# Optimization experiments

Hardware: AMD Instinct MI355X
Metric: run time of the kernel (lower is better)

## Reference

```python
import jax, jax.numpy as jnp
import numpy as np

N = 50000        # nodes
E = 1_600_000    # edges (avg degree 32)
IN_DIM = 128
NUM_CONFS = 16
CONF_EMB = 4
HIDDEN = 64
OUT = 32


def setup_inputs() -> dict:
    key = jax.random.key(0)
    ks = jax.random.split(key, 8)
    x = jax.random.normal(ks[0], (N, IN_DIM), jnp.float32)
    conf_ids = jax.random.randint(ks[1], (N,), 0, NUM_CONFS)
    edge_index = jax.random.randint(ks[2], (2, E), 0, N)
    edge_weight = jax.random.uniform(ks[3], (E,), jnp.float32)
    # learned params
    conf_table = jax.random.normal(ks[4], (NUM_CONFS, CONF_EMB), jnp.float32) * 0.1
    W1 = jax.random.normal(ks[5], (IN_DIM + CONF_EMB, HIDDEN), jnp.float32) / np.sqrt(IN_DIM + CONF_EMB)
    b1 = jnp.zeros((HIDDEN,), jnp.float32)
    W2 = jax.random.normal(ks[6], (HIDDEN, OUT), jnp.float32) / np.sqrt(HIDDEN)
    b2 = jnp.zeros((OUT,), jnp.float32)
    return dict(x=x, conf_ids=conf_ids, edge_index=edge_index, edge_weight=edge_weight,
                conf_table=conf_table, W1=W1, b1=b1, W2=W2, b2=b2)


def _gcn_conv(h, W, b, row, col, w, n):
    """PyG GCNConv: symmetric norm with self-loops (loops already appended to row/col/w)."""
    deg = jax.ops.segment_sum(w, col, num_segments=n)              # weighted in-degree [N]
    dinv = jnp.where(deg > 0, jax.lax.rsqrt(deg), 0.0)             # D^{-1/2}
    norm = dinv[row] * w * dinv[col]                               # per-edge coefficient [E+N]
    hW = h @ W                                                     # [N, out]
    out = jax.ops.segment_sum(hW[row] * norm[:, None], col, num_segments=n)
    return out + b


def reference(x, conf_ids, edge_index, edge_weight, conf_table, W1, b1, W2, b2):
    row, col = edge_index[0], edge_index[1]
    # add self-loops once (same math for both conv layers)
    loop = jnp.arange(N)
    row = jnp.concatenate([row, loop])
    col = jnp.concatenate([col, loop])
    w = jnp.concatenate([edge_weight, jnp.ones((N,), edge_weight.dtype)])

    h = jnp.concatenate([x, conf_table[conf_ids]], axis=-1)        # [N, in+conf_emb]
    h = jax.nn.relu(_gcn_conv(h, W1, b1, row, col, w, N))
    return _gcn_conv(h, W2, b2, row, col, w, N)
```

## Files before the change

### kernel.cpp

```cpp
#include <hip/hip_runtime.h>
#include <hip/hip_fp16.h>

#define BKT_SHIFT 8
#define BKT_SIZE  256
#define SEGCAP    12544
#define EPB       4096
#define EPT       16
#define NTX       64

__global__ void k_zero(int* __restrict__ cursor) {
    cursor[threadIdx.x] = 0;
}

__global__ void k_binA(const int* __restrict__ row, const int* __restrict__ col,
                       const float* __restrict__ w, int* __restrict__ cursor,
                       uint2* __restrict__ seg, int e) {
    __shared__ int hist[256];
    __shared__ int begL[256];
    __shared__ int gbase[256];
    __shared__ int rank[256];
    __shared__ uint2 pay[EPB];
    int t = threadIdx.x;
    hist[t] = 0; rank[t] = 0;
    __syncthreads();
    int b0 = blockIdx.x * EPB;
    int cnt_local = min(EPB, e - b0);
    unsigned pv[EPT]; unsigned cc[EPT];
#pragma unroll
    for (int k = 0; k < EPT; ++k) {
        int i = b0 + k * 256 + t;
        if (i < e) {
            unsigned r  = (unsigned)row[i];
            unsigned c  = (unsigned)col[i];
            unsigned wq = (unsigned)__half_as_ushort(__float2half_rn(w[i]));
            pv[k] = r | (wq << 16);
            cc[k] = c;
            atomicAdd(&hist[c >> BKT_SHIFT], 1);
        } else cc[k] = 0xFFFFFFFFu;
    }
    __syncthreads();
    int v = hist[t];
    begL[t] = v;
    __syncthreads();
    for (int off = 1; off < 256; off <<= 1) {
        int tv = (t >= off) ? begL[t - off] : 0;
        __syncthreads();
        begL[t] += tv;
        __syncthreads();
    }
    int excl = begL[t] - v;
    __syncthreads();
    begL[t] = excl;
    if (v > 0) gbase[t] = atomicAdd(&cursor[t], v);
    __syncthreads();
#pragma unroll
    for (int k = 0; k < EPT; ++k) {
        if (cc[k] != 0xFFFFFFFFu) {
            int b = cc[k] >> BKT_SHIFT;
            int pos = begL[b] + atomicAdd(&rank[b], 1);
            pay[pos] = make_uint2(pv[k], ((unsigned)b << 8) | (cc[k] & (BKT_SIZE - 1)));
        }
    }
    __syncthreads();
    for (int i = t; i < cnt_local; i += 256) {
        uint2 r = pay[i];
        int b = r.y >> 8;
        int gidx = gbase[b] + (i - begL[b]);
        if (gidx < SEGCAP)
            seg[(size_t)b * SEGCAP + gidx] = make_uint2(r.x, r.y & (BKT_SIZE - 1));
    }
}

__global__ void k_binB(const int* __restrict__ cursor, const uint2* __restrict__ seg,
                       unsigned* __restrict__ csr, int* __restrict__ begs,
                       int* __restrict__ cnts, float* __restrict__ dinv, int n) {
    __shared__ int hist[BKT_SIZE];
    __shared__ float wsumf[BKT_SIZE];
    __shared__ int begL[BKT_SIZE];
    __shared__ int rank[BKT_SIZE];
    __shared__ unsigned pay[SEGCAP];
    int b = blockIdx.x;
    int t = threadIdx.x;
    int nodes = min(BKT_SIZE, n - b * BKT_SIZE);
    int count = min(cursor[b], SEGCAP);
    hist[t] = 0; wsumf[t] = 0.f; rank[t] = 0;
    __syncthreads();
    const uint2* sp = seg + (size_t)b * SEGCAP;
    for (int i = t; i < count; i += 256) {
        uint2 r = sp[i];
        atomicAdd(&hist[r.y], 1);
        atomicAdd(&wsumf[r.y], __half2float(__ushort_as_half((unsigned short)(r.x >> 16))));
    }
    __syncthreads();
    int v = hist[t];
    int vpad = (v + 15) & ~15;
    begL[t] = vpad;
    __syncthreads();
    for (int off = 1; off < 256; off <<= 1) {
        int tv = (t >= off) ? begL[t - off] : 0;
        __syncthreads();
        begL[t] += tv;
        __syncthreads();
    }
    int beg_excl = begL[t] - vpad;
    int ptot = min(begL[255], SEGCAP);
    __syncthreads();
    begL[t] = beg_excl;
    if (t < nodes) {
        int node = b * BKT_SIZE + t;
        begs[node] = b * SEGCAP + beg_excl;
        cnts[node] = vpad;
        dinv[node] = rsqrtf(1.0f + wsumf[t]);
    }
    for (int i = t; i < ptot; i += 256) pay[i] = 0u;
    __syncthreads();
    for (int i = t; i < count; i += 256) {
        uint2 r = sp[i];
        int pos = begL[r.y] + atomicAdd(&rank[r.y], 1);
        if (pos < SEGCAP) pay[pos] = r.x;
    }
    __syncthreads();
    unsigned* cp = csr + (size_t)b * SEGCAP;
    for (int i = t; i < ptot; i += 256) cp[i] = pay[i];
}

__global__ void k_hw1(const float* __restrict__ x, const int* __restrict__ conf_ids,
                      const float* __restrict__ conf_table, const float* __restrict__ W1,
                      const float* __restrict__ dinv, __half* __restrict__ hW1s, int n) {
    __shared__ float xs[NTX][132];
    int t = threadIdx.x;
    int base = blockIdx.x * NTX;
    for (int q = t; q < NTX * 32; q += 256) {
        int node = base + (q >> 5);
        int k4 = (q & 31) * 4;
        float4 v = make_float4(0.f, 0.f, 0.f, 0.f);
        if (node < n) v = *(const float4*)(x + (size_t)node * 128 + k4);
        *(float4*)&xs[q >> 5][k4] = v;
    }
    if (t < NTX) {
        int node = base + t;
        int cid = (node < n) ? conf_ids[node] : 0;
        float4 ce = *(const float4*)(conf_table + cid * 4);
        if (node >= n) ce = make_float4(0.f, 0.f, 0.f, 0.f);
        *(float4*)&xs[t][128] = ce;
    }
    __syncthreads();
    int w = t >> 6;
    int lane = t & 63;
    int fbase = __builtin_amdgcn_readfirstlane(w * 16);
    const float* __restrict__ wp = W1 + fbase;
    float acc[16];
#pragma unroll
    for (int j = 0; j < 16; ++j) acc[j] = 0.f;
    for (int k4 = 0; k4 < 132; k4 += 4) {
        float4 xv = *(const float4*)&xs[lane][k4];
#pragma unroll
        for (int j = 0; j < 16; ++j) {
            acc[j] += xv.x * wp[(k4 + 0) * 64 + j]
                    + xv.y * wp[(k4 + 1) * 64 + j]
                    + xv.z * wp[(k4 + 2) * 64 + j]
                    + xv.w * wp[(k4 + 3) * 64 + j];
        }
    }
    int node = base + lane;
    if (node < n) {
        float dn = dinv[node];
        half2* hp = (half2*)(hW1s + (size_t)node * 64 + fbase);
#pragma unroll
        for (int j = 0; j < 8; ++j)
            hp[j] = __floats2half2_rn(acc[2 * j] * dn, acc[2 * j + 1] * dn);
    }
}

__global__ void k_agg1(const __half* __restrict__ hW1s, const int* __restrict__ begs,
                       const int* __restrict__ cnts, const unsigned* __restrict__ csr,
                       const float* __restrict__ dinv, const float* __restrict__ b1,
                       const float* __restrict__ W2, __half* __restrict__ hW2s, int n) {
    __shared__ float h1s[8][64];
    int t = threadIdx.x;
    int q  = t >> 5;
    int hl = t & 31;
    int nid = blockIdx.x * 8 + q;
    const half2* __restrict__ hrow = (const half2*)hW1s;
    float dn = 0.f;
    float2 sf = make_float2(0.f, 0.f);
    int c = 0;
    const unsigned* sp = csr;
    if (nid < n) {
        dn = dinv[nid];
        c = cnts[nid];
        sp = csr + begs[nid];
        sf = __half22float2(hrow[(size_t)nid * 32 + hl]);
    }
    float a0 = 0.f, a1 = 0.f;
    const half2 hz = __float2half2_rn(0.f);
    uint4 s0 = *(const uint4*)(sp);
    uint4 s1 = *(const uint4*)(sp + 4);
    uint4 s2 = *(const uint4*)(sp + 8);
    uint4 s3 = *(const uint4*)(sp + 12);
    for (int j = 0; j < c; j += 16) {
        uint4 n0 = *(const uint4*)(sp + j + 16);
        uint4 n1 = *(const uint4*)(sp + j + 20);
        uint4 n2 = *(const uint4*)(sp + j + 24);
        uint4 n3 = *(const uint4*)(sp + j + 28);
        half2 acc0 = hz, acc1 = hz, acc2 = hz, acc3 = hz;
#define STEP1(s, A) { half2 vv = hrow[(size_t)((s) & 0xffffu) * 32 + hl]; \
                      half2 ww = __half2half2(__ushort_as_half((unsigned short)((s) >> 16))); \
                      A = __hfma2(vv, ww, A); }
        STEP1(s0.x, acc0) STEP1(s0.y, acc1) STEP1(s0.z, acc2) STEP1(s0.w, acc3)
        STEP1(s1.x, acc0) STEP1(s1.y, acc1) STEP1(s1.z, acc2) STEP1(s1.w, acc3)
        STEP1(s2.x, acc0) STEP1(s2.y, acc1) STEP1(s2.z, acc2) STEP1(s2.w, acc3)
        STEP1(s3.x, acc0) STEP1(s3.y, acc1) STEP1(s3.z, acc2) STEP1(s3.w, acc3)
#undef STEP1
        float2 f0 = __half22float2(acc0);
        float2 f1 = __half22float2(acc1);
        float2 f2 = __half22float2(acc2);
        float2 f3 = __half22float2(acc3);
        a0 += (f0.x + f1.x) + (f2.x + f3.x);
        a1 += (f0.y + f1.y) + (f2.y + f3.y);
        s0 = n0; s1 = n1; s2 = n2; s3 = n3;
    }
    float2 bb = *(const float2*)(b1 + 2 * hl);
    float h0  = fmaxf((sf.x + a0) * dn + bb.x, 0.0f);
    float h1v = fmaxf((sf.y + a1) * dn + bb.y, 0.0f);
    if (nid >= n) { h0 = 0.f; h1v = 0.f; }
    *(float2*)&h1s[q][2 * hl] = make_float2(h0, h1v);
    __syncthreads();
    float s = 0.f;
#pragma unroll
    for (int k = 0; k < 64; k += 4) {
        float4 hv = *(const float4*)&h1s[q][k];
        s += hv.x * W2[(k + 0) * 32 + hl];
        s += hv.y * W2[(k + 1) * 32 + hl];
        s += hv.z * W2[(k + 2) * 32 + hl];
        s += hv.w * W2[(k + 3) * 32 + hl];
    }
    if (nid < n) hW2s[(size_t)nid * 32 + hl] = __float2half_rn(s * dn);
}

__global__ void k_agg2(const __half* __restrict__ hW2s, const int* __restrict__ begs,
                       const int* __restrict__ cnts, const unsigned* __restrict__ csr,
                       const float* __restrict__ dinv, const float* __restrict__ b2,
                       float* __restrict__ out, int n) {
    int t = threadIdx.x;
    int g  = t >> 4;
    int hl = t & 15;
    int nid = blockIdx.x * 16 + g;
    const half2* __restrict__ hrow = (const half2*)hW2s;
    float dn = 0.f;
    float2 sf = make_float2(0.f, 0.f);
    int c = 0;
    const unsigned* sp = csr;
    if (nid < n) {
        dn = dinv[nid];
        c = cnts[nid];
        sp = csr + begs[nid];
        sf = __half22float2(hrow[(size_t)nid * 16 + hl]);
    }
    float a0 = 0.f, a1 = 0.f;
    const half2 hz = __float2half2_rn(0.f);
    uint4 s0 = *(const uint4*)(sp);
    uint4 s1 = *(const uint4*)(sp + 4);
    uint4 s2 = *(const uint4*)(sp + 8);
    uint4 s3 = *(const uint4*)(sp + 12);
    for (int j = 0; j < c; j += 16) {
        uint4 n0 = *(const uint4*)(sp + j + 16);
        uint4 n1 = *(const uint4*)(sp + j + 20);
        uint4 n2 = *(const uint4*)(sp + j + 24);
        uint4 n3 = *(const uint4*)(sp + j + 28);
        half2 acc0 = hz, acc1 = hz, acc2 = hz, acc3 = hz;
#define STEP2(s, A) { half2 vv = hrow[(size_t)((s) & 0xffffu) * 16 + hl]; \
                      half2 ww = __half2half2(__ushort_as_half((unsigned short)((s) >> 16))); \
                      A = __hfma2(vv, ww, A); }
        STEP2(s0.x, acc0) STEP2(s0.y, acc1) STEP2(s0.z, acc2) STEP2(s0.w, acc3)
        STEP2(s1.x, acc0) STEP2(s1.y, acc1) STEP2(s1.z, acc2) STEP2(s1.w, acc3)
        STEP2(s2.x, acc0) STEP2(s2.y, acc1) STEP2(s2.z, acc2) STEP2(s2.w, acc3)
        STEP2(s3.x, acc0) STEP2(s3.y, acc1) STEP2(s3.z, acc2) STEP2(s3.w, acc3)
#undef STEP2
        float2 f0 = __half22float2(acc0);
        float2 f1 = __half22float2(acc1);
        float2 f2 = __half22float2(acc2);
        float2 f3 = __half22float2(acc3);
        a0 += (f0.x + f1.x) + (f2.x + f3.x);
        a1 += (f0.y + f1.y) + (f2.y + f3.y);
        s0 = n0; s1 = n1; s2 = n2; s3 = n3;
    }
    if (nid < n) {
        float2 bb = *(const float2*)(b2 + 2 * hl);
        float o0 = (sf.x + a0) * dn + bb.x;
        float o1 = (sf.y + a1) * dn + bb.y;
        *(float2*)&out[(size_t)nid * 32 + 2 * hl] = make_float2(o0, o1);
    }
}

extern "C" void kernel_launch(void* const* d_in, const int* in_sizes, int n_in,
                              void* d_out, int out_size, void* d_ws, size_t ws_size,
                              hipStream_t stream) {
    const float* x          = (const float*)d_in[0];
    const int*   conf_ids   = (const int*)  d_in[1];
    const int*   eidx       = (const int*)  d_in[2];
    const float* ew         = (const float*)d_in[3];
    const float* conf_table = (const float*)d_in[4];
    const float* W1         = (const float*)d_in[5];
    const float* b1         = (const float*)d_in[6];
    const float* W2         = (const float*)d_in[7];
    const float* b2         = (const float*)d_in[8];
    float* out = (float*)d_out;

    const int n = in_sizes[1];
    const int e = in_sizes[3];
    const int* row = eidx;
    const int* col = eidx + e;
    const int nbkt = (n + BKT_SIZE - 1) / BKT_SIZE;

    char* ws = (char*)d_ws;
    size_t off = 0;
    auto alloc = [&](size_t bytes) -> char* {
        char* p = ws + off;
        off = (off + bytes + 255) & ~(size_t)255;
        return p;
    };
    int*      cursor = (int*)     alloc(256 * 4);
    uint2*    seg    = (uint2*)   alloc((size_t)nbkt * SEGCAP * 8);
    unsigned* csr    = (unsigned*)alloc((size_t)nbkt * SEGCAP * 4);
    int*      begs   = (int*)     alloc((size_t)n * 4);
    int*      cnts   = (int*)     alloc((size_t)n * 4);
    float*    dinv   = (float*)   alloc((size_t)n * 4);
    __half*   hW2s   = (__half*)  alloc((size_t)n * 32 * 2);
    __half*   hW1s   = (__half*)  alloc((size_t)n * 64 * 2);

    const int B = 256;
    int ga  = (e + EPB - 1) / EPB;
    int gt  = (n + NTX - 1) / NTX;
    int g8  = (n + 7) / 8;
    int g16 = (n + 15) / 16;

    k_zero<<<1,    B, 0, stream>>>(cursor);
    k_binA<<<ga,   B, 0, stream>>>(row, col, ew, cursor, seg, e);
    k_binB<<<nbkt, B, 0, stream>>>(cursor, seg, csr, begs, cnts, dinv, n);
    k_hw1 <<<gt,   B, 0, stream>>>(x, conf_ids, conf_table, W1, dinv, hW1s, n);
    k_agg1<<<g8,   B, 0, stream>>>(hW1s, begs, cnts, csr, dinv, b1, W2, hW2s, n);
    k_agg2<<<g16,  B, 0, stream>>>(hW2s, begs, cnts, csr, dinv, b2, out, n);
}
```

Before: 121.6 us.

## Run X·W1 GEMM concurrently with edge binning and apply dinv scaling in binB

Merges the edge-binning kernel and the dense X·W1 kernel into one launch, with blocks split by blockIdx, so the GEMM no longer waits for degree computation and can overlap with binning. The dinv row scaling moves into k_binB, which rescales the unscaled fp16 hW1 rows of its bucket after computing dinv. This removes one launch and the serial dependency, but adds an extra read-modify-write pass over hW1 and a second fp16 rounding step. The shared-memory union sizes each block to the larger of the two layouts, which may lower occupancy for the GEMM blocks.

```diff
diff --git a/kernel.cpp b/kernel.cpp
--- a/kernel.cpp
+++ b/kernel.cpp
@@ -12,68 +12,116 @@
     cursor[threadIdx.x] = 0;
 }
 
-__global__ void k_binA(const int* __restrict__ row, const int* __restrict__ col,
-                       const float* __restrict__ w, int* __restrict__ cursor,
-                       uint2* __restrict__ seg, int e) {
-    __shared__ int hist[256];
-    __shared__ int begL[256];
-    __shared__ int gbase[256];
-    __shared__ int rank[256];
-    __shared__ uint2 pay[EPB];
+struct ShA { int hist[256]; int begL[256]; int gbase[256]; int rank[256]; uint2 pay[EPB]; };
+struct ShH { float xs[NTX][132]; };
+
+__global__ void k_binA_hw1(const int* __restrict__ row, const int* __restrict__ col,
+                           const float* __restrict__ w, int* __restrict__ cursor,
+                           uint2* __restrict__ seg,
+                           const float* __restrict__ x, const int* __restrict__ conf_ids,
+                           const float* __restrict__ conf_table, const float* __restrict__ W1,
+                           __half* __restrict__ hW1, int e, int n, int ga) {
+    __shared__ __align__(16) char raw[sizeof(ShA) > sizeof(ShH) ? sizeof(ShA) : sizeof(ShH)];
     int t = threadIdx.x;
-    hist[t] = 0; rank[t] = 0;
-    __syncthreads();
-    int b0 = blockIdx.x * EPB;
-    int cnt_local = min(EPB, e - b0);
-    unsigned pv[EPT]; unsigned cc[EPT];
-#pragma unroll
-    for (int k = 0; k < EPT; ++k) {
-        int i = b0 + k * 256 + t;
-        if (i < e) {
-            unsigned r  = (unsigned)row[i];
-            unsigned c  = (unsigned)col[i];
-            unsigned wq = (unsigned)__half_as_ushort(__float2half_rn(w[i]));
-            pv[k] = r | (wq << 16);
-            cc[k] = c;
-            atomicAdd(&hist[c >> BKT_SHIFT], 1);
-        } else cc[k] = 0xFFFFFFFFu;
-    }
-    __syncthreads();
-    int v = hist[t];
-    begL[t] = v;
-    __syncthreads();
-    for (int off = 1; off < 256; off <<= 1) {
-        int tv = (t >= off) ? begL[t - off] : 0;
-        __syncthreads();
-        begL[t] += tv;
-        __syncthreads();
-    }
-    int excl = begL[t] - v;
-    __syncthreads();
-    begL[t] = excl;
-    if (v > 0) gbase[t] = atomicAdd(&cursor[t], v);
-    __syncthreads();
-#pragma unroll
-    for (int k = 0; k < EPT; ++k) {
-        if (cc[k] != 0xFFFFFFFFu) {
-            int b = cc[k] >> BKT_SHIFT;
-            int pos = begL[b] + atomicAdd(&rank[b], 1);
-            pay[pos] = make_uint2(pv[k], ((unsigned)b << 8) | (cc[k] & (BKT_SIZE - 1)));
-        }
-    }
-    __syncthreads();
-    for (int i = t; i < cnt_local; i += 256) {
-        uint2 r = pay[i];
-        int b = r.y >> 8;
-        int gidx = gbase[b] + (i - begL[b]);
-        if (gidx < SEGCAP)
-            seg[(size_t)b * SEGCAP + gidx] = make_uint2(r.x, r.y & (BKT_SIZE - 1));
+    if ((int)blockIdx.x < ga) {
+        ShA& A = *reinterpret_cast<ShA*>(raw);
+        A.hist[t] = 0; A.rank[t] = 0;
+        __syncthreads();
+        int b0 = blockIdx.x * EPB;
+        int cnt_local = min(EPB, e - b0);
+        unsigned pv[EPT]; unsigned cc[EPT];
+#pragma unroll
+        for (int k = 0; k < EPT; ++k) {
+            int i = b0 + k * 256 + t;
+            if (i < e) {
+                unsigned r  = (unsigned)row[i];
+                unsigned c  = (unsigned)col[i];
+                unsigned wq = (unsigned)__half_as_ushort(__float2half_rn(w[i]));
+                pv[k] = r | (wq << 16);
+                cc[k] = c;
+                atomicAdd(&A.hist[c >> BKT_SHIFT], 1);
+            } else cc[k] = 0xFFFFFFFFu;
+        }
+        __syncthreads();
+        int v = A.hist[t];
+        A.begL[t] = v;
+        __syncthreads();
+        for (int off = 1; off < 256; off <<= 1) {
+            int tv = (t >= off) ? A.begL[t - off] : 0;
+            __syncthreads();
+            A.begL[t] += tv;
+            __syncthreads();
+        }
+        int excl = A.begL[t] - v;
+        __syncthreads();
+        A.begL[t] = excl;
+        if (v > 0) A.gbase[t] = atomicAdd(&cursor[t], v);
+        __syncthreads();
+#pragma unroll
+        for (int k = 0; k < EPT; ++k) {
+            if (cc[k] != 0xFFFFFFFFu) {
+                int b = cc[k] >> BKT_SHIFT;
+                int pos = A.begL[b] + atomicAdd(&A.rank[b], 1);
+                A.pay[pos] = make_uint2(pv[k], ((unsigned)b << 8) | (cc[k] & (BKT_SIZE - 1)));
+            }
+        }
+        __syncthreads();
+        for (int i = t; i < cnt_local; i += 256) {
+            uint2 r = A.pay[i];
+            int b = r.y >> 8;
+            int gidx = A.gbase[b] + (i - A.begL[b]);
+            if (gidx < SEGCAP)
+                seg[(size_t)b * SEGCAP + gidx] = make_uint2(r.x, r.y & (BKT_SIZE - 1));
+        }
+    } else {
+        ShH& H = *reinterpret_cast<ShH*>(raw);
+        int base = (blockIdx.x - ga) * NTX;
+        for (int q = t; q < NTX * 32; q += 256) {
+            int node = base + (q >> 5);
+            int k4 = (q & 31) * 4;
+            float4 v = make_float4(0.f, 0.f, 0.f, 0.f);
+            if (node < n) v = *(const float4*)(x + (size_t)node * 128 + k4);
+            *(float4*)&H.xs[q >> 5][k4] = v;
+        }
+        if (t < NTX) {
+            int node = base + t;
+            int cid = (node < n) ? conf_ids[node] : 0;
+            float4 ce = *(const float4*)(conf_table + cid * 4);
+            if (node >= n) ce = make_float4(0.f, 0.f, 0.f, 0.f);
+            *(float4*)&H.xs[t][128] = ce;
+        }
+        __syncthreads();
+        int wv = t >> 6;
+        int lane = t & 63;
+        int fbase = __builtin_amdgcn_readfirstlane(wv * 16);
+        const float* __restrict__ wp = W1 + fbase;
+        float acc[16];
+#pragma unroll
+        for (int j = 0; j < 16; ++j) acc[j] = 0.f;
+        for (int k4 = 0; k4 < 132; k4 += 4) {
+            float4 xv = *(const float4*)&H.xs[lane][k4];
+#pragma unroll
+            for (int j = 0; j < 16; ++j) {
+                acc[j] += xv.x * wp[(k4 + 0) * 64 + j]
+                        + xv.y * wp[(k4 + 1) * 64 + j]
+                        + xv.z * wp[(k4 + 2) * 64 + j]
+                        + xv.w * wp[(k4 + 3) * 64 + j];
+            }
+        }
+        int node = base + lane;
+        if (node < n) {
+            half2* hp = (half2*)(hW1 + (size_t)node * 64 + fbase);
+#pragma unroll
+            for (int j = 0; j < 8; ++j)
+                hp[j] = __floats2half2_rn(acc[2 * j], acc[2 * j + 1]);
+        }
     }
 }
 
 __global__ void k_binB(const int* __restrict__ cursor, const uint2* __restrict__ seg,
                        unsigned* __restrict__ csr, int* __restrict__ begs,
-                       int* __restrict__ cnts, float* __restrict__ dinv, int n) {
+                       int* __restrict__ cnts, float* __restrict__ dinv,
+                       __half* __restrict__ hW1, int n) {
     __shared__ int hist[BKT_SIZE];
     __shared__ float wsumf[BKT_SIZE];
     __shared__ int begL[BKT_SIZE];
@@ -106,11 +154,14 @@
     int ptot = min(begL[255], SEGCAP);
     __syncthreads();
     begL[t] = beg_excl;
+    float dv = rsqrtf(1.0f + wsumf[t]);
+    __syncthreads();
+    wsumf[t] = dv;
     if (t < nodes) {
         int node = b * BKT_SIZE + t;
         begs[node] = b * SEGCAP + beg_excl;
         cnts[node] = vpad;
-        dinv[node] = rsqrtf(1.0f + wsumf[t]);
+        dinv[node] = dv;
     }
     for (int i = t; i < ptot; i += 256) pay[i] = 0u;
     __syncthreads();
@@ -122,53 +173,12 @@
     __syncthreads();
     unsigned* cp = csr + (size_t)b * SEGCAP;
     for (int i = t; i < ptot; i += 256) cp[i] = pay[i];
-}
-
-__global__ void k_hw1(const float* __restrict__ x, const int* __restrict__ conf_ids,
-                      const float* __restrict__ conf_table, const float* __restrict__ W1,
-                      const float* __restrict__ dinv, __half* __restrict__ hW1s, int n) {
-    __shared__ float xs[NTX][132];
-    int t = threadIdx.x;
-    int base = blockIdx.x * NTX;
-    for (int q = t; q < NTX * 32; q += 256) {
-        int node = base + (q >> 5);
-        int k4 = (q & 31) * 4;
-        float4 v = make_float4(0.f, 0.f, 0.f, 0.f);
-        if (node < n) v = *(const float4*)(x + (size_t)node * 128 + k4);
-        *(float4*)&xs[q >> 5][k4] = v;
-    }
-    if (t < NTX) {
-        int node = base + t;
-        int cid = (node < n) ? conf_ids[node] : 0;
-        float4 ce = *(const float4*)(conf_table + cid * 4);
-        if (node >= n) ce = make_float4(0.f, 0.f, 0.f, 0.f);
-        *(float4*)&xs[t][128] = ce;
-    }
-    __syncthreads();
-    int w = t >> 6;
-    int lane = t & 63;
-    int fbase = __builtin_amdgcn_readfirstlane(w * 16);
-    const float* __restrict__ wp = W1 + fbase;
-    float acc[16];
-#pragma unroll
-    for (int j = 0; j < 16; ++j) acc[j] = 0.f;
-    for (int k4 = 0; k4 < 132; k4 += 4) {
-        float4 xv = *(const float4*)&xs[lane][k4];
-#pragma unroll
-        for (int j = 0; j < 16; ++j) {
-            acc[j] += xv.x * wp[(k4 + 0) * 64 + j]
-                    + xv.y * wp[(k4 + 1) * 64 + j]
-                    + xv.z * wp[(k4 + 2) * 64 + j]
-                    + xv.w * wp[(k4 + 3) * 64 + j];
-        }
-    }
-    int node = base + lane;
-    if (node < n) {
-        float dn = dinv[node];
-        half2* hp = (half2*)(hW1s + (size_t)node * 64 + fbase);
-#pragma unroll
-        for (int j = 0; j < 8; ++j)
-            hp[j] = __floats2half2_rn(acc[2 * j] * dn, acc[2 * j + 1] * dn);
+    half2* hp = (half2*)(hW1 + (size_t)b * BKT_SIZE * 64);
+    int lim = nodes * 32;
+    for (int i = t; i < lim; i += 256) {
+        float dn = wsumf[i >> 5];
+        float2 f = __half22float2(hp[i]);
+        hp[i] = __floats2half2_rn(f.x * dn, f.y * dn);
     }
 }
 
@@ -327,7 +337,7 @@
     int*      cnts   = (int*)     alloc((size_t)n * 4);
     float*    dinv   = (float*)   alloc((size_t)n * 4);
     __half*   hW2s   = (__half*)  alloc((size_t)n * 32 * 2);
-    __half*   hW1s   = (__half*)  alloc((size_t)n * 64 * 2);
+    __half*   hW1    = (__half*)  alloc((size_t)n * 64 * 2);
 
     const int B = 256;
     int ga  = (e + EPB - 1) / EPB;
@@ -335,10 +345,10 @@
     int g8  = (n + 7) / 8;
     int g16 = (n + 15) / 16;
 
-    k_zero<<<1,    B, 0, stream>>>(cursor);
-    k_binA<<<ga,   B, 0, stream>>>(row, col, ew, cursor, seg, e);
-    k_binB<<<nbkt, B, 0, stream>>>(cursor, seg, csr, begs, cnts, dinv, n);
-    k_hw1 <<<gt,   B, 0, stream>>>(x, conf_ids, conf_table, W1, dinv, hW1s, n);
-    k_agg1<<<g8,   B, 0, stream>>>(hW1s, begs, cnts, csr, dinv, b1, W2, hW2s, n);
-    k_agg2<<<g16,  B, 0, stream>>>(hW2s, begs, cnts, csr, dinv, b2, out, n);
-}
+    k_zero    <<<1,       B, 0, stream>>>(cursor);
+    k_binA_hw1<<<ga + gt, B, 0, stream>>>(row, col, ew, cursor, seg,
+                                          x, conf_ids, conf_table, W1, hW1, e, n, ga);
+    k_binB    <<<nbkt,    B, 0, stream>>>(cursor, seg, csr, begs, cnts, dinv, hW1, n);
+    k_agg1    <<<g8,      B, 0, stream>>>(hW1, begs, cnts, csr, dinv, b1, W2, hW2s, n);
+    k_agg2    <<<g16,     B, 0, stream>>>(hW2s, begs, cnts, csr, dinv, b2, out, n);
+}
```

Result: no change. 122.8 us (+1.0%).

## Reorder dense transform before binning, pad cursors, use wave-shuffle scan in binA

Applied to the files above, without the earlier changes.

k_hw1 now runs before k_binB and no longer depends on dinv. k_binB applies the dinv scaling to hW1 in place, which breaks the dependency and gives more freedom in kernel ordering. binA now uses half the edges per block to launch more blocks, and its block scan uses wave shuffles instead of barrier loops. The global cursor counters are spread out with a stride so that contended atomics sit on separate cache lines. The cost is an extra read and write of hW1 inside binB, and the pairs rounding twice to fp16.

```diff
diff --git a/kernel.cpp b/kernel.cpp
--- a/kernel.cpp
+++ b/kernel.cpp
@@ -4,12 +4,13 @@
 #define BKT_SHIFT 8
 #define BKT_SIZE  256
 #define SEGCAP    12544
-#define EPB       4096
-#define EPT       16
+#define EPB       2048
+#define EPT       8
 #define NTX       64
+#define CSTR      32
 
 __global__ void k_zero(int* __restrict__ cursor) {
-    cursor[threadIdx.x] = 0;
+    for (int i = threadIdx.x; i < 256 * CSTR; i += 256) cursor[i] = 0;
 }
 
 __global__ void k_binA(const int* __restrict__ row, const int* __restrict__ col,
@@ -19,6 +20,7 @@
     __shared__ int begL[256];
     __shared__ int gbase[256];
     __shared__ int rank[256];
+    __shared__ int wsum[4];
     __shared__ uint2 pay[EPB];
     int t = threadIdx.x;
     hist[t] = 0; rank[t] = 0;
@@ -40,18 +42,21 @@
     }
     __syncthreads();
     int v = hist[t];
-    begL[t] = v;
-    __syncthreads();
-    for (int off = 1; off < 256; off <<= 1) {
-        int tv = (t >= off) ? begL[t - off] : 0;
-        __syncthreads();
-        begL[t] += tv;
-        __syncthreads();
-    }
-    int excl = begL[t] - v;
-    __syncthreads();
+    int lane = t & 63, wid = t >> 6;
+    int s = v;
+#pragma unroll
+    for (int off = 1; off < 64; off <<= 1) {
+        int u = __shfl_up(s, off);
+        if (lane >= off) s += u;
+    }
+    if (lane == 63) wsum[wid] = s;
+    __syncthreads();
+    int pre = 0;
+#pragma unroll
+    for (int k = 0; k < 4; ++k) if (k < wid) pre += wsum[k];
+    int excl = s + pre - v;
     begL[t] = excl;
-    if (v > 0) gbase[t] = atomicAdd(&cursor[t], v);
+    if (v > 0) gbase[t] = atomicAdd(&cursor[t * CSTR], v);
     __syncthreads();
 #pragma unroll
     for (int k = 0; k < EPT; ++k) {
@@ -71,62 +76,9 @@
     }
 }
 
-__global__ void k_binB(const int* __restrict__ cursor, const uint2* __restrict__ seg,
-                       unsigned* __restrict__ csr, int* __restrict__ begs,
-                       int* __restrict__ cnts, float* __restrict__ dinv, int n) {
-    __shared__ int hist[BKT_SIZE];
-    __shared__ float wsumf[BKT_SIZE];
-    __shared__ int begL[BKT_SIZE];
-    __shared__ int rank[BKT_SIZE];
-    __shared__ unsigned pay[SEGCAP];
-    int b = blockIdx.x;
-    int t = threadIdx.x;
-    int nodes = min(BKT_SIZE, n - b * BKT_SIZE);
-    int count = min(cursor[b], SEGCAP);
-    hist[t] = 0; wsumf[t] = 0.f; rank[t] = 0;
-    __syncthreads();
-    const uint2* sp = seg + (size_t)b * SEGCAP;
-    for (int i = t; i < count; i += 256) {
-        uint2 r = sp[i];
-        atomicAdd(&hist[r.y], 1);
-        atomicAdd(&wsumf[r.y], __half2float(__ushort_as_half((unsigned short)(r.x >> 16))));
-    }
-    __syncthreads();
-    int v = hist[t];
-    int vpad = (v + 15) & ~15;
-    begL[t] = vpad;
-    __syncthreads();
-    for (int off = 1; off < 256; off <<= 1) {
-        int tv = (t >= off) ? begL[t - off] : 0;
-        __syncthreads();
-        begL[t] += tv;
-        __syncthreads();
-    }
-    int beg_excl = begL[t] - vpad;
-    int ptot = min(begL[255], SEGCAP);
-    __syncthreads();
-    begL[t] = beg_excl;
-    if (t < nodes) {
-        int node = b * BKT_SIZE + t;
-        begs[node] = b * SEGCAP + beg_excl;
-        cnts[node] = vpad;
-        dinv[node] = rsqrtf(1.0f + wsumf[t]);
-    }
-    for (int i = t; i < ptot; i += 256) pay[i] = 0u;
-    __syncthreads();
-    for (int i = t; i < count; i += 256) {
-        uint2 r = sp[i];
-        int pos = begL[r.y] + atomicAdd(&rank[r.y], 1);
-        if (pos < SEGCAP) pay[pos] = r.x;
-    }
-    __syncthreads();
-    unsigned* cp = csr + (size_t)b * SEGCAP;
-    for (int i = t; i < ptot; i += 256) cp[i] = pay[i];
-}
-
 __global__ void k_hw1(const float* __restrict__ x, const int* __restrict__ conf_ids,
                       const float* __restrict__ conf_table, const float* __restrict__ W1,
-                      const float* __restrict__ dinv, __half* __restrict__ hW1s, int n) {
+                      __half* __restrict__ hW1, int n) {
     __shared__ float xs[NTX][132];
     int t = threadIdx.x;
     int base = blockIdx.x * NTX;
@@ -145,9 +97,9 @@
         *(float4*)&xs[t][128] = ce;
     }
     __syncthreads();
-    int w = t >> 6;
+    int wv = t >> 6;
     int lane = t & 63;
-    int fbase = __builtin_amdgcn_readfirstlane(w * 16);
+    int fbase = __builtin_amdgcn_readfirstlane(wv * 16);
     const float* __restrict__ wp = W1 + fbase;
     float acc[16];
 #pragma unroll
@@ -164,11 +116,74 @@
     }
     int node = base + lane;
     if (node < n) {
-        float dn = dinv[node];
-        half2* hp = (half2*)(hW1s + (size_t)node * 64 + fbase);
+        half2* hp = (half2*)(hW1 + (size_t)node * 64 + fbase);
 #pragma unroll
         for (int j = 0; j < 8; ++j)
-            hp[j] = __floats2half2_rn(acc[2 * j] * dn, acc[2 * j + 1] * dn);
+            hp[j] = __floats2half2_rn(acc[2 * j], acc[2 * j + 1]);
+    }
+}
+
+__global__ void k_binB(const int* __restrict__ cursor, const uint2* __restrict__ seg,
+                       unsigned* __restrict__ csr, int* __restrict__ begs,
+                       int* __restrict__ cnts, float* __restrict__ dinv,
+                       __half* __restrict__ hW1, int n) {
+    __shared__ int hist[BKT_SIZE];
+    __shared__ float wsumf[BKT_SIZE];
+    __shared__ int begL[BKT_SIZE];
+    __shared__ int rank[BKT_SIZE];
+    __shared__ unsigned pay[SEGCAP];
+    int b = blockIdx.x;
+    int t = threadIdx.x;
+    int nodes = min(BKT_SIZE, n - b * BKT_SIZE);
+    int count = min(cursor[b * CSTR], SEGCAP);
+    hist[t] = 0; wsumf[t] = 0.f; rank[t] = 0;
+    __syncthreads();
+    const uint2* sp = seg + (size_t)b * SEGCAP;
+    for (int i = t; i < count; i += 256) {
+        uint2 r = sp[i];
+        atomicAdd(&hist[r.y], 1);
+        atomicAdd(&wsumf[r.y], __half2float(__ushort_as_half((unsigned short)(r.x >> 16))));
+    }
+    __syncthreads();
+    int v = hist[t];
+    int vpad = (v + 15) & ~15;
+    begL[t] = vpad;
+    __syncthreads();
+    for (int off = 1; off < 256; off <<= 1) {
+        int tv = (t >= off) ? begL[t - off] : 0;
+        __syncthreads();
+        begL[t] += tv;
+        __syncthreads();
+    }
+    int beg_excl = begL[t] - vpad;
+    int ptot = min(begL[255], SEGCAP);
+    __syncthreads();
+    begL[t] = beg_excl;
+    float dv = rsqrtf(1.0f + wsumf[t]);
+    __syncthreads();
+    wsumf[t] = dv;
+    if (t < nodes) {
+        int node = b * BKT_SIZE + t;
+        begs[node] = b * SEGCAP + beg_excl;
+        cnts[node] = vpad;
+        dinv[node] = dv;
+    }
+    for (int i = t; i < ptot; i += 256) pay[i] = 0u;
+    __syncthreads();
+    for (int i = t; i < count; i += 256) {
+        uint2 r = sp[i];
+        int pos = begL[r.y] + atomicAdd(&rank[r.y], 1);
+        if (pos < SEGCAP) pay[pos] = r.x;
+    }
+    __syncthreads();
+    unsigned* cp = csr + (size_t)b * SEGCAP;
+    for (int i = t; i < ptot; i += 256) cp[i] = pay[i];
+    half2* hp = (half2*)(hW1 + (size_t)b * BKT_SIZE * 64);
+    int lim = nodes * 32;
+    for (int i = t; i < lim; i += 256) {
+        float dn = wsumf[i >> 5];
+        float2 f = __half22float2(hp[i]);
+        hp[i] = __floats2half2_rn(f.x * dn, f.y * dn);
     }
 }
 
@@ -320,14 +335,14 @@
         off = (off + bytes + 255) & ~(size_t)255;
         return p;
     };
-    int*      cursor = (int*)     alloc(256 * 4);
+    int*      cursor = (int*)     alloc(256 * CSTR * 4);
     uint2*    seg    = (uint2*)   alloc((size_t)nbkt * SEGCAP * 8);
     unsigned* csr    = (unsigned*)alloc((size_t)nbkt * SEGCAP * 4);
     int*      begs   = (int*)     alloc((size_t)n * 4);
     int*      cnts   = (int*)     alloc((size_t)n * 4);
     float*    dinv   = (float*)   alloc((size_t)n * 4);
     __half*   hW2s   = (__half*)  alloc((size_t)n * 32 * 2);
-    __half*   hW1s   = (__half*)  alloc((size_t)n * 64 * 2);
+    __half*   hW1    = (__half*)  alloc((size_t)n * 64 * 2);
 
     const int B = 256;
     int ga  = (e + EPB - 1) / EPB;
@@ -337,8 +352,8 @@
 
     k_zero<<<1,    B, 0, stream>>>(cursor);
     k_binA<<<ga,   B, 0, stream>>>(row, col, ew, cursor, seg, e);
-    k_binB<<<nbkt, B, 0, stream>>>(cursor, seg, csr, begs, cnts, dinv, n);
-    k_hw1 <<<gt,   B, 0, stream>>>(x, conf_ids, conf_table, W1, dinv, hW1s, n);
-    k_agg1<<<g8,   B, 0, stream>>>(hW1s, begs, cnts, csr, dinv, b1, W2, hW2s, n);
+    k_hw1 <<<gt,   B, 0, stream>>>(x, conf_ids, conf_table, W1, hW1, n);
+    k_binB<<<nbkt, B, 0, stream>>>(cursor, seg, csr, begs, cnts, dinv, hW1, n);
+    k_agg1<<<g8,   B, 0, stream>>>(hW1, begs, cnts, csr, dinv, b1, W2, hW2s, n);
     k_agg2<<<g16,  B, 0, stream>>>(hW2s, begs, cnts, csr, dinv, b2, out, n);
 }
```

Result: slower. 126.9 us (+4.4%).

## Fuse cursor zeroing into hW1 GEMM and apply dinv scaling inside binB

Applied to the files above, without the earlier changes.

Moves the feature transform x·W1 to the start of the pipeline, merged with cursor zeroing, so it no longer depends on dinv and the separate k_zero launch goes away. The dinv row scaling is applied afterwards in k_binB, which reads back each bucket's hW1 rows, scales them and rewrites them in fp16. This removes one kernel launch but adds an extra read-modify-write pass over hW1 and rounds to fp16 twice.

```diff
diff --git a/kernel.cpp b/kernel.cpp
--- a/kernel.cpp
+++ b/kernel.cpp
@@ -8,8 +8,52 @@
 #define EPT       16
 #define NTX       64
 
-__global__ void k_zero(int* __restrict__ cursor) {
-    cursor[threadIdx.x] = 0;
+__global__ void k_hw1z(const float* __restrict__ x, const int* __restrict__ conf_ids,
+                       const float* __restrict__ conf_table, const float* __restrict__ W1,
+                       __half* __restrict__ hW1, int* __restrict__ cursor, int n) {
+    __shared__ float xs[NTX][132];
+    int t = threadIdx.x;
+    if (blockIdx.x == 0) cursor[t] = 0;
+    int base = blockIdx.x * NTX;
+    for (int q = t; q < NTX * 32; q += 256) {
+        int node = base + (q >> 5);
+        int k4 = (q & 31) * 4;
+        float4 v = make_float4(0.f, 0.f, 0.f, 0.f);
+        if (node < n) v = *(const float4*)(x + (size_t)node * 128 + k4);
+        *(float4*)&xs[q >> 5][k4] = v;
+    }
+    if (t < NTX) {
+        int node = base + t;
+        int cid = (node < n) ? conf_ids[node] : 0;
+        float4 ce = *(const float4*)(conf_table + cid * 4);
+        if (node >= n) ce = make_float4(0.f, 0.f, 0.f, 0.f);
+        *(float4*)&xs[t][128] = ce;
+    }
+    __syncthreads();
+    int wv = t >> 6;
+    int lane = t & 63;
+    int fbase = __builtin_amdgcn_readfirstlane(wv * 16);
+    const float* __restrict__ wp = W1 + fbase;
+    float acc[16];
+#pragma unroll
+    for (int j = 0; j < 16; ++j) acc[j] = 0.f;
+    for (int k4 = 0; k4 < 132; k4 += 4) {
+        float4 xv = *(const float4*)&xs[lane][k4];
+#pragma unroll
+        for (int j = 0; j < 16; ++j) {
+            acc[j] += xv.x * wp[(k4 + 0) * 64 + j]
+                    + xv.y * wp[(k4 + 1) * 64 + j]
+                    + xv.z * wp[(k4 + 2) * 64 + j]
+                    + xv.w * wp[(k4 + 3) * 64 + j];
+        }
+    }
+    int node = base + lane;
+    if (node < n) {
+        half2* hp = (half2*)(hW1 + (size_t)node * 64 + fbase);
+#pragma unroll
+        for (int j = 0; j < 8; ++j)
+            hp[j] = __floats2half2_rn(acc[2 * j], acc[2 * j + 1]);
+    }
 }
 
 __global__ void k_binA(const int* __restrict__ row, const int* __restrict__ col,
@@ -73,7 +117,8 @@
 
 __global__ void k_binB(const int* __restrict__ cursor, const uint2* __restrict__ seg,
                        unsigned* __restrict__ csr, int* __restrict__ begs,
-                       int* __restrict__ cnts, float* __restrict__ dinv, int n) {
+                       int* __restrict__ cnts, float* __restrict__ dinv,
+                       __half* __restrict__ hW1, int n) {
     __shared__ int hist[BKT_SIZE];
     __shared__ float wsumf[BKT_SIZE];
     __shared__ int begL[BKT_SIZE];
@@ -106,11 +151,14 @@
     int ptot = min(begL[255], SEGCAP);
     __syncthreads();
     begL[t] = beg_excl;
+    float dv = rsqrtf(1.0f + wsumf[t]);
+    __syncthreads();
+    wsumf[t] = dv;
     if (t < nodes) {
         int node = b * BKT_SIZE + t;
         begs[node] = b * SEGCAP + beg_excl;
         cnts[node] = vpad;
-        dinv[node] = rsqrtf(1.0f + wsumf[t]);
+        dinv[node] = dv;
     }
     for (int i = t; i < ptot; i += 256) pay[i] = 0u;
     __syncthreads();
@@ -122,53 +170,12 @@
     __syncthreads();
     unsigned* cp = csr + (size_t)b * SEGCAP;
     for (int i = t; i < ptot; i += 256) cp[i] = pay[i];
-}
-
-__global__ void k_hw1(const float* __restrict__ x, const int* __restrict__ conf_ids,
-                      const float* __restrict__ conf_table, const float* __restrict__ W1,
-                      const float* __restrict__ dinv, __half* __restrict__ hW1s, int n) {
-    __shared__ float xs[NTX][132];
-    int t = threadIdx.x;
-    int base = blockIdx.x * NTX;
-    for (int q = t; q < NTX * 32; q += 256) {
-        int node = base + (q >> 5);
-        int k4 = (q & 31) * 4;
-        float4 v = make_float4(0.f, 0.f, 0.f, 0.f);
-        if (node < n) v = *(const float4*)(x + (size_t)node * 128 + k4);
-        *(float4*)&xs[q >> 5][k4] = v;
-    }
-    if (t < NTX) {
-        int node = base + t;
-        int cid = (node < n) ? conf_ids[node] : 0;
-        float4 ce = *(const float4*)(conf_table + cid * 4);
-        if (node >= n) ce = make_float4(0.f, 0.f, 0.f, 0.f);
-        *(float4*)&xs[t][128] = ce;
-    }
-    __syncthreads();
-    int w = t >> 6;
-    int lane = t & 63;
-    int fbase = __builtin_amdgcn_readfirstlane(w * 16);
-    const float* __restrict__ wp = W1 + fbase;
-    float acc[16];
-#pragma unroll
-    for (int j = 0; j < 16; ++j) acc[j] = 0.f;
-    for (int k4 = 0; k4 < 132; k4 += 4) {
-        float4 xv = *(const float4*)&xs[lane][k4];
-#pragma unroll
-        for (int j = 0; j < 16; ++j) {
-            acc[j] += xv.x * wp[(k4 + 0) * 64 + j]
-                    + xv.y * wp[(k4 + 1) * 64 + j]
-                    + xv.z * wp[(k4 + 2) * 64 + j]
-                    + xv.w * wp[(k4 + 3) * 64 + j];
-        }
-    }
-    int node = base + lane;
-    if (node < n) {
-        float dn = dinv[node];
-        half2* hp = (half2*)(hW1s + (size_t)node * 64 + fbase);
-#pragma unroll
-        for (int j = 0; j < 8; ++j)
-            hp[j] = __floats2half2_rn(acc[2 * j] * dn, acc[2 * j + 1] * dn);
+    half2* hp = (half2*)(hW1 + (size_t)b * BKT_SIZE * 64);
+    int lim = nodes * 32;
+    for (int i = t; i < lim; i += 256) {
+        float dn = wsumf[i >> 5];
+        float2 f = __half22float2(hp[i]);
+        hp[i] = __floats2half2_rn(f.x * dn, f.y * dn);
     }
 }
 
@@ -327,7 +334,7 @@
     int*      cnts   = (int*)     alloc((size_t)n * 4);
     float*    dinv   = (float*)   alloc((size_t)n * 4);
     __half*   hW2s   = (__half*)  alloc((size_t)n * 32 * 2);
-    __half*   hW1s   = (__half*)  alloc((size_t)n * 64 * 2);
+    __half*   hW1    = (__half*)  alloc((size_t)n * 64 * 2);
 
     const int B = 256;
     int ga  = (e + EPB - 1) / EPB;
@@ -335,10 +342,9 @@
     int g8  = (n + 7) / 8;
     int g16 = (n + 15) / 16;
 
-    k_zero<<<1,    B, 0, stream>>>(cursor);
+    k_hw1z<<<gt,   B, 0, stream>>>(x, conf_ids, conf_table, W1, hW1, cursor, n);
     k_binA<<<ga,   B, 0, stream>>>(row, col, ew, cursor, seg, e);
-    k_binB<<<nbkt, B, 0, stream>>>(cursor, seg, csr, begs, cnts, dinv, n);
-    k_hw1 <<<gt,   B, 0, stream>>>(x, conf_ids, conf_table, W1, dinv, hW1s, n);
-    k_agg1<<<g8,   B, 0, stream>>>(hW1s, begs, cnts, csr, dinv, b1, W2, hW2s, n);
+    k_binB<<<nbkt, B, 0, stream>>>(cursor, seg, csr, begs, cnts, dinv, hW1, n);
+    k_agg1<<<g8,   B, 0, stream>>>(hW1, begs, cnts, csr, dinv, b1, W2, hW2s, n);
     k_agg2<<<g16,  B, 0, stream>>>(hW2s, begs, cnts, csr, dinv, b2, out, n);
 }
```

Result: slower. 125.4 us (+3.1%).
